# Optimization experiments

Measured on AMD Instinct MI355X. Metric: run time of the kernel, lower is better.

## Reference

```python
import jax, jax.numpy as jnp
import numpy as np

B, T, F, H, E = 256, 512, 32, 512, 32
NUM_TICKERS, PREDICT_DAYS = 5000, 30


def setup_inputs() -> dict:
    key = jax.random.key(0)
    ks = jax.random.split(key, 16)
    s = 0.05  # small init scale for stability
    return {
        "ticker_id": jax.random.randint(ks[0], (B,), 0, NUM_TICKERS),
        "sequence": jax.random.normal(ks[1], (B, T, F), jnp.float32),
        "embed_table": jax.random.normal(ks[2], (NUM_TICKERS, E), jnp.float32) * s,
        "Wih0": jax.random.normal(ks[3], (3 * H, F), jnp.float32) * s,
        "Whh0": jax.random.normal(ks[4], (3 * H, H), jnp.float32) * s,
        "bih0": jax.random.normal(ks[5], (3 * H,), jnp.float32) * s,
        "bhh0": jax.random.normal(ks[6], (3 * H,), jnp.float32) * s,
        "Wih1": jax.random.normal(ks[7], (3 * H, H), jnp.float32) * s,
        "Whh1": jax.random.normal(ks[8], (3 * H, H), jnp.float32) * s,
        "bih1": jax.random.normal(ks[9], (3 * H,), jnp.float32) * s,
        "bhh1": jax.random.normal(ks[10], (3 * H,), jnp.float32) * s,
        "fc1_w": jax.random.normal(ks[11], (H, H + E), jnp.float32) * s,
        "fc1_b": jax.random.normal(ks[12], (H,), jnp.float32) * s,
        "fc2_w": jax.random.normal(ks[13], (PREDICT_DAYS, H), jnp.float32) * s,
        "fc2_b": jax.random.normal(ks[14], (PREDICT_DAYS,), jnp.float32) * s,
    }


def _gru_layer(x, Wih, Whh, bih, bhh):
    """Standard torch-convention GRU layer. x: (B,T,in) -> (B,T,H), h_last (B,H).
    Gate packing along 3H axis: [r, z, n]."""
    Hs = Whh.shape[1]
    # precompute input projections for all timesteps in one GEMM
    gx = jnp.einsum('btf,gf->tbg', x, Wih) + bih  # (T,B,3H)

    def step(h, gxt):
        gh = h @ Whh.T + bhh                         # (B,3H)
        r = jax.nn.sigmoid(gxt[:, :Hs] + gh[:, :Hs])
        z = jax.nn.sigmoid(gxt[:, Hs:2 * Hs] + gh[:, Hs:2 * Hs])
        n = jnp.tanh(gxt[:, 2 * Hs:] + r * gh[:, 2 * Hs:])
        h_new = (1.0 - z) * n + z * h
        return h_new, h_new

    h0 = jnp.zeros((x.shape[0], Hs), x.dtype)
    h_last, ys = jax.lax.scan(step, h0, gx)          # ys: (T,B,H)
    return jnp.moveaxis(ys, 0, 1), h_last


def reference(ticker_id, sequence, embed_table, Wih0, Whh0, bih0, bhh0,
              Wih1, Whh1, bih1, bhh1, fc1_w, fc1_b, fc2_w, fc2_b):
    out0, _ = _gru_layer(sequence, Wih0, Whh0, bih0, bhh0)
    _, h_last = _gru_layer(out0, Wih1, Whh1, bih1, bhh1)   # top-layer final hidden (B,H)
    embed = embed_table[ticker_id]                          # (B,E)
    h = jnp.concatenate([h_last, embed], axis=1)            # (B,H+E)
    h = jax.nn.relu(h @ fc1_w.T + fc1_b)                    # dropout is eval no-op
    return h @ fc2_w.T + fc2_b                              # (B, predict_days)
```

## Files before the change

### kernel.cpp

```cpp
#include <hip/hip_runtime.h>
#include <hip/hip_bf16.h>


namespace {
constexpr int kB  = 256;
constexpr int kT  = 512;
constexpr int kF  = 32;
constexpr int kH  = 512;
constexpr int kE  = 32;
constexpr int kPD = 30;

constexpr int GBLK = 256;
constexpr int NTHR = 256;
constexpr int RG   = 32;
constexpr int HB   = 16;

constexpr int IMG  = kB * kH * 2;
constexpr int RING = 8;

constexpr int PART_OFF = 0;
constexpr int MB_OFF   = 8192;
constexpr int LDSB     = 98304;
static_assert(LDSB <= 160 * 1024, "LDS overflow");

constexpr size_t WS_CNT   = 0;
constexpr size_t WS_TOTAL = 1024;
constexpr size_t WS_FB    = 1152;
constexpr size_t WS_FLG   = 2048;
constexpr size_t WS_H0B   = 65536;
constexpr size_t WS_H1B   = WS_H0B + (size_t)RING * IMG;
constexpr size_t WS_H1F   = WS_H1B + (size_t)RING * IMG;
constexpr size_t WS_INIT  = WS_H1F;

typedef __bf16 bf16_t;
typedef __bf16 bf16x8 __attribute__((ext_vector_type(8)));
typedef float  f32x4  __attribute__((ext_vector_type(4)));

#define MFMA __builtin_amdgcn_mfma_f32_16x16x32_bf16
#define LDSF4(p) (*(__attribute__((address_space(3))) f32x4*)(p))
#define LDSVU(p) (*(volatile __attribute__((address_space(3))) unsigned*)(p))

#define WAITVM(N)                                              \
  do {                                                         \
    asm volatile("s_waitcnt vmcnt(" #N ")" ::: "memory");      \
    __builtin_amdgcn_sched_barrier(0);                         \
  } while (0)

__device__ __forceinline__ float sigmoid_f(float x) {
  return 1.f / (1.f + __expf(-x));
}
__device__ __forceinline__ float tanh_f(float x) {
  float a = fabsf(x);
  float e = __expf(-2.f * a);
  float t = (1.f - e) / (1.f + e);
  return copysignf(t, x);
}

__device__ __forceinline__ bf16x8 ld16a(const char* p) {
  bf16x8 v;
  asm volatile("global_load_dwordx4 %0, %1, off"
               : "=v"(v) : "v"(p) : "memory");
  return v;
}

__device__ __forceinline__ bf16x8 fragf(const float* p) {
  bf16x8 t;
#pragma unroll
  for (int j = 0; j < 8; ++j) t[j] = (bf16_t)p[j];
  return t;
}

__device__ __forceinline__ bf16x8 ld16_mall(const bf16_t* p) {
  const unsigned long long* q = (const unsigned long long*)p;
  unsigned long long lo =
      __hip_atomic_load(q, __ATOMIC_RELAXED, __HIP_MEMORY_SCOPE_AGENT);
  unsigned long long hi =
      __hip_atomic_load(q + 1, __ATOMIC_RELAXED, __HIP_MEMORY_SCOPE_AGENT);
  union { unsigned long long u[2]; bf16x8 v; } x;
  x.u[0] = lo; x.u[1] = hi;
  return x.v;
}

__device__ __forceinline__ void st2_mall(bf16_t* p, float v) {
  bf16_t b = (bf16_t)v;
  unsigned short bits = __builtin_bit_cast(unsigned short, b);
  __hip_atomic_store((unsigned short*)p, bits, __ATOMIC_RELAXED,
                     __HIP_MEMORY_SCOPE_AGENT);
}
template <bool XL>
__device__ __forceinline__ void st2x(bf16_t* p, float v) {
  if constexpr (XL) *p = (bf16_t)v;
  else st2_mall(p, v);
}

__device__ __forceinline__ void drain_stores() {
  asm volatile("s_waitcnt vmcnt(0)" ::: "memory");
}

__device__ __forceinline__ void busy_fma(float* a) {
#pragma unroll
  for (int i = 0; i < 16; ++i) {
    asm volatile("v_fmac_f32 %0, %1, %2" : "+v"(a[0]) : "v"(a[1]), "v"(a[2]));
    asm volatile("v_fmac_f32 %0, %1, %2" : "+v"(a[1]) : "v"(a[2]), "v"(a[3]));
    asm volatile("v_fmac_f32 %0, %1, %2" : "+v"(a[2]) : "v"(a[3]), "v"(a[0]));
    asm volatile("v_fmac_f32 %0, %1, %2" : "+v"(a[3]) : "v"(a[0]), "v"(a[1]));
  }
}

__device__ __forceinline__ void mb_spin(unsigned* mbp, unsigned tgt,
                                        float* a) {
  long guard = 0;
  while (LDSVU(mbp) < tgt) {
    busy_fma(a);
    if (++guard > (1L << 20)) break;
  }
  asm volatile("" ::: "memory");
}

__device__ __forceinline__ unsigned ld_flag_sc1(const unsigned* p) {
  unsigned v;
  asm volatile("global_load_dword %0, %1, off sc1\n\ts_waitcnt vmcnt(0)"
               : "=v"(v) : "v"(p) : "memory");
  return v;
}

template <bool XL>
__device__ __forceinline__ void flag_store(unsigned* flgp, int slot,
                                           unsigned tgt) {
  if constexpr (XL) {
    *(volatile unsigned*)(flgp + slot) = tgt;
  } else {
    __hip_atomic_store(flgp + slot, tgt, __ATOMIC_RELAXED,
                       __HIP_MEMORY_SCOPE_AGENT);
  }
}

template <bool XL>
__device__ __forceinline__ void flag_poll(const unsigned* flgp, int lane,
                                          unsigned tgt) {
  const unsigned* fp = flgp + (lane & 31);
  long guard = 0;
  if constexpr (XL) {
    for (;;) {
      unsigned v = ld_flag_sc1(fp);
      if (__all((int)(v >= tgt))) break;
      if (++guard > (1L << 22)) break;
    }
  } else {
    for (;;) {
      unsigned v = __hip_atomic_load(fp, __ATOMIC_RELAXED,
                                     __HIP_MEMORY_SCOPE_AGENT);
      if (__all((int)(v >= tgt))) break;
      __builtin_amdgcn_s_sleep(1);
      if (++guard > (1L << 20)) break;
    }
  }
}
}


#define L0_ISSUE(buf, base)                                         \
  _Pragma("unroll") for (int j = 0; j < 4; ++j)                     \
      buf[j] = ld16a(hsrc + (base + j) * 1024)
#define L0_MFMA(buf, base)                                          \
  _Pragma("unroll") for (int j = 0; j < 4; ++j) {                   \
    aR  = MFMA(buf[j], f0[0][base + j], aR, 0, 0, 0);               \
    aZ  = MFMA(buf[j], f0[1][base + j], aZ, 0, 0, 0);               \
    aNH = MFMA(buf[j], f0[2][base + j], aNH, 0, 0, 0);              \
  }
#define L1_ISSUE(b0, b1, base)                                      \
  _Pragma("unroll") for (int j = 0; j < 4; ++j) {                   \
    b0[j] = ld16a(hsrc + (base + j) * 1024);                        \
    b1[j] = ld16a(hsrc + 16384 + (base + j) * 1024);                \
  }
#define L1_MFMA(acc0, acc1, acc2, w, b0, b1, base)                  \
  _Pragma("unroll") for (int j = 0; j < 4; ++j) {                   \
    acc0[0] = MFMA(b0[j], w[0][base + j], acc0[0], 0, 0, 0);        \
    acc0[1] = MFMA(b1[j], w[0][base + j], acc0[1], 0, 0, 0);        \
    acc1[0] = MFMA(b0[j], w[1][base + j], acc1[0], 0, 0, 0);        \
    acc1[1] = MFMA(b1[j], w[1][base + j], acc1[1], 0, 0, 0);        \
    acc2[0] = MFMA(b0[j], w[2][base + j], acc2[0], 0, 0, 0);        \
    acc2[1] = MFMA(b1[j], w[2][base + j], acc2[1], 0, 0, 0);        \
  }

template <bool XL>
__device__ __attribute__((noinline)) void role_l0(
    const float* __restrict__ seq, const float* __restrict__ Whh0,
    const float* __restrict__ Wih0, bf16_t* __restrict__ h0b,
    unsigned* mbp, int g, int slot, int lane, int rbase, int rt, int c,
    float b0r, float b0z, float b0nx, float b0nh) {
  const int lm = lane & 15, lq = lane >> 4, koff = lq * 8;
  const int arow = rbase + rt * 16 + lm;

  bf16x8 f0[3][17];
#pragma unroll
  for (int gg = 0; gg < 3; ++gg) {
    const float* wh = Whh0 + (size_t)(gg * kH + c) * kH + koff;
#pragma unroll
    for (int kc = 0; kc < 16; ++kc) f0[gg][kc] = fragf(wh + kc * 32);
    f0[gg][16] = fragf(Wih0 + (size_t)(gg * kH + c) * kF + koff);
  }
  float h0m[4] = {0.f, 0.f, 0.f, 0.f};
  float spin[4] = {1.0f + lane, 0.5f, 0.25f, 0.125f};

  const int kcb = slot >> 1;
  const int lq2 = ((slot & 1) << 1) | (lm >> 3);
  const int stoff = ((g * 2 + rt) * 16 + kcb) * 1024 +
                    ((lq2 << 4) + lq * 4) * 16 + (lm & 7) * 2;
  const int tbase = (g * 2 + rt) * 16 * 1024;

  for (int s = 0; s <= kT; ++s) {
    const int pr = (s + RING - 1) & (RING - 1), pw = s & (RING - 1);
    if (s < kT) {
      f32x4 aR{0,0,0,0}, aZ{0,0,0,0}, aNH{0,0,0,0}, aNX{0,0,0,0};
      const char* hsrc = (const char*)h0b + pr * IMG + tbase + lane * 16;
      const float* xp = seq + ((size_t)arow * kT + s) * kF + koff;
      float xs[8];
#pragma unroll
      for (int j = 0; j < 8; ++j) xs[j] = xp[j];
      if constexpr (XL) {
        bf16x8 cA[4], cB[4];
        L0_ISSUE(cA, 0);
        L0_ISSUE(cB, 4);
        WAITVM(4);
        L0_MFMA(cA, 0);
        L0_ISSUE(cA, 8);
        WAITVM(4);
        L0_MFMA(cB, 4);
        L0_ISSUE(cB, 12);
        WAITVM(4);
        L0_MFMA(cA, 8);
        WAITVM(0);
        L0_MFMA(cB, 12);
      } else {
#pragma unroll
        for (int kc = 0; kc < 16; ++kc) {
          bf16x8 a = ld16_mall((const bf16_t*)(hsrc + kc * 1024));
          aR  = MFMA(a, f0[0][kc], aR, 0, 0, 0);
          aZ  = MFMA(a, f0[1][kc], aZ, 0, 0, 0);
          aNH = MFMA(a, f0[2][kc], aNH, 0, 0, 0);
        }
      }
      {
        bf16x8 ax;
#pragma unroll
        for (int j = 0; j < 8; ++j) ax[j] = (bf16_t)xs[j];
        aR  = MFMA(ax, f0[0][16], aR, 0, 0, 0);
        aZ  = MFMA(ax, f0[1][16], aZ, 0, 0, 0);
        aNX = MFMA(ax, f0[2][16], aNX, 0, 0, 0);
      }
      char* hnb = (char*)h0b + pw * IMG;
#pragma unroll
      for (int i = 0; i < 4; ++i) {
        float r = sigmoid_f(aR[i] + b0r);
        float z = sigmoid_f(aZ[i] + b0z);
        float n = tanh_f((aNX[i] + b0nx) + r * (aNH[i] + b0nh));
        float hn = (1.f - z) * n + z * h0m[i];
        h0m[i] = hn;
        st2x<XL>((bf16_t*)(hnb + stoff + i * 16), hn);
      }
    }
    __syncthreads();
    if constexpr (XL) {
      if (s < kT) mb_spin(mbp, (unsigned)(s + 1), spin);
    } else {
      __syncthreads();
    }
  }
}

template <bool XL>
__device__ __attribute__((noinline)) void role_l1h(
    const float* __restrict__ Whh1, bf16_t* __restrict__ h1b,
    float* __restrict__ h1f, unsigned* __restrict__ flgp, int slot,
    float* part, unsigned* mbp, int g, int lane, int rbase, int c,
    float b1r, float b1z, float b1nx, float b1nh) {
  const int lm = lane & 15, lq = lane >> 4, koff = lq * 8;
  bf16x8 fh[3][16];
#pragma unroll
  for (int gg = 0; gg < 3; ++gg) {
    const float* wh = Whh1 + (size_t)(gg * kH + c) * kH + koff;
#pragma unroll
    for (int kc = 0; kc < 16; ++kc) fh[gg][kc] = fragf(wh + kc * 32);
  }
  float h1m[2][4] = {{0,0,0,0},{0,0,0,0}};

  const int kcb = slot >> 1;
  const int lq2 = ((slot & 1) << 1) | (lm >> 3);
  const int st0 = (g * 2 * 16 + kcb) * 1024 +
                  ((lq2 << 4) + lq * 4) * 16 + (lm & 7) * 2;
  const int tbase = g * 2 * 16 * 1024;

  for (int s = 0; s <= kT; ++s) {
    const int pr = (s + RING - 1) & (RING - 1), pw = s & (RING - 1);
    f32x4 cR[2], cZ[2], cNH[2];
#pragma unroll
    for (int rt = 0; rt < 2; ++rt) {
      cR[rt] = f32x4{0,0,0,0}; cZ[rt] = f32x4{0,0,0,0}; cNH[rt] = f32x4{0,0,0,0};
    }
    if (s >= 1) {
      const char* hsrc = (const char*)h1b + pr * IMG + tbase + lane * 16;
      if constexpr (XL) {
        bf16x8 a0A[4], a1A[4], a0B[4], a1B[4];
        L1_ISSUE(a0A, a1A, 0);
        L1_ISSUE(a0B, a1B, 4);
        WAITVM(8);
        L1_MFMA(cR, cZ, cNH, fh, a0A, a1A, 0);
        L1_ISSUE(a0A, a1A, 8);
        WAITVM(8);
        L1_MFMA(cR, cZ, cNH, fh, a0B, a1B, 4);
        L1_ISSUE(a0B, a1B, 12);
        WAITVM(8);
        L1_MFMA(cR, cZ, cNH, fh, a0A, a1A, 8);
        WAITVM(0);
        L1_MFMA(cR, cZ, cNH, fh, a0B, a1B, 12);
      } else {
#pragma unroll
        for (int kc = 0; kc < 16; ++kc) {
          bf16x8 a0 = ld16_mall((const bf16_t*)(hsrc + kc * 1024));
          bf16x8 a1 = ld16_mall((const bf16_t*)(hsrc + 16384 + kc * 1024));
          cR[0]  = MFMA(a0, fh[0][kc], cR[0], 0,0,0);
          cR[1]  = MFMA(a1, fh[0][kc], cR[1], 0,0,0);
          cZ[0]  = MFMA(a0, fh[1][kc], cZ[0], 0,0,0);
          cZ[1]  = MFMA(a1, fh[1][kc], cZ[1], 0,0,0);
          cNH[0] = MFMA(a0, fh[2][kc], cNH[0],0,0,0);
          cNH[1] = MFMA(a1, fh[2][kc], cNH[1],0,0,0);
        }
      }
    }
    __syncthreads();
    if (s >= 1) {
      char* hnb = (char*)h1b + pw * IMG;
#pragma unroll
      for (int rt = 0; rt < 2; ++rt) {
        f32x4 pR  = LDSF4(part + ((rt * 3 + 0) * 64 + lane) * 4);
        f32x4 pZ  = LDSF4(part + ((rt * 3 + 1) * 64 + lane) * 4);
        f32x4 pNX = LDSF4(part + ((rt * 3 + 2) * 64 + lane) * 4);
#pragma unroll
        for (int i = 0; i < 4; ++i) {
          float r = sigmoid_f(cR[rt][i] + pR[i] + b1r);
          float z = sigmoid_f(cZ[rt][i] + pZ[i] + b1z);
          float n = tanh_f((pNX[i] + b1nx) + r * (cNH[rt][i] + b1nh));
          float hn = (1.f - z) * n + z * h1m[rt][i];
          h1m[rt][i] = hn;
          if (s < kT) st2x<XL>((bf16_t*)(hnb + st0 + rt * 16384 + i * 16), hn);
          else        h1f[(rbase + rt * 16 + lq * 4 + i) * kH + c] = hn;
        }
      }
    }
    if constexpr (XL) {
      if (s < kT) {
        drain_stores();
        if (lane == 0) flag_store<XL>(flgp, slot, (unsigned)(s + 1));
        flag_poll<XL>(flgp, lane, (unsigned)(s + 1));
        if ((s & (RING - 1)) == (RING - 1))
          asm volatile("buffer_inv" ::: "memory");
        if (lane == 0) LDSVU(mbp) = (unsigned)(s + 1);
      }
    } else {
      if (s < kT) {
        drain_stores();
        if (lane == 0) flag_store<XL>(flgp, slot, (unsigned)(s + 1));
        flag_poll<XL>(flgp, lane, (unsigned)(s + 1));
      }
      __syncthreads();
    }
  }
}

template <bool XL>
__device__ __attribute__((noinline)) void role_l1x(
    const float* __restrict__ Wih1, bf16_t* __restrict__ h0b,
    float* part, unsigned* mbp, int g, int lane, int c) {
  const int lq = lane >> 4, koff = lq * 8;
  bf16x8 fx[3][16];
#pragma unroll
  for (int gg = 0; gg < 3; ++gg) {
    const float* wi = Wih1 + (size_t)(gg * kH + c) * kH + koff;
#pragma unroll
    for (int kc = 0; kc < 16; ++kc) fx[gg][kc] = fragf(wi + kc * 32);
  }
  const int tbase = g * 2 * 16 * 1024;
  float spin[4] = {3.0f + lane, 0.5f, 0.25f, 0.125f};

  for (int s = 0; s <= kT; ++s) {
    const int pr = (s + RING - 1) & (RING - 1);
    if (s >= 1) {
      f32x4 xR[2], xZ[2], xNX[2];
#pragma unroll
      for (int rt = 0; rt < 2; ++rt) {
        xR[rt] = f32x4{0,0,0,0}; xZ[rt] = f32x4{0,0,0,0}; xNX[rt] = f32x4{0,0,0,0};
      }
      const char* hsrc = (const char*)h0b + pr * IMG + tbase + lane * 16;
      if constexpr (XL) {
        bf16x8 a0A[4], a1A[4], a0B[4], a1B[4];
        L1_ISSUE(a0A, a1A, 0);
        L1_ISSUE(a0B, a1B, 4);
        WAITVM(8);
        L1_MFMA(xR, xZ, xNX, fx, a0A, a1A, 0);
        L1_ISSUE(a0A, a1A, 8);
        WAITVM(8);
        L1_MFMA(xR, xZ, xNX, fx, a0B, a1B, 4);
        L1_ISSUE(a0B, a1B, 12);
        WAITVM(8);
        L1_MFMA(xR, xZ, xNX, fx, a0A, a1A, 8);
        WAITVM(0);
        L1_MFMA(xR, xZ, xNX, fx, a0B, a1B, 12);
      } else {
#pragma unroll
        for (int kc = 0; kc < 16; ++kc) {
          bf16x8 a0 = ld16_mall((const bf16_t*)(hsrc + kc * 1024));
          bf16x8 a1 = ld16_mall((const bf16_t*)(hsrc + 16384 + kc * 1024));
          xR[0]  = MFMA(a0, fx[0][kc], xR[0], 0,0,0);
          xR[1]  = MFMA(a1, fx[0][kc], xR[1], 0,0,0);
          xZ[0]  = MFMA(a0, fx[1][kc], xZ[0], 0,0,0);
          xZ[1]  = MFMA(a1, fx[1][kc], xZ[1], 0,0,0);
          xNX[0] = MFMA(a0, fx[2][kc], xNX[0],0,0,0);
          xNX[1] = MFMA(a1, fx[2][kc], xNX[1],0,0,0);
        }
      }
#pragma unroll
      for (int rt = 0; rt < 2; ++rt) {
        LDSF4(part + ((rt * 3 + 0) * 64 + lane) * 4) = xR[rt];
        LDSF4(part + ((rt * 3 + 1) * 64 + lane) * 4) = xZ[rt];
        LDSF4(part + ((rt * 3 + 2) * 64 + lane) * 4) = xNX[rt];
      }
    }
    __syncthreads();
    if constexpr (XL) {
      if (s < kT) mb_spin(mbp, (unsigned)(s + 1), spin);
    } else {
      __syncthreads();
    }
  }
}

__launch_bounds__(NTHR, 1)
__global__ void gru_persistent(
    const float* __restrict__ seq,
    const float* __restrict__ Wih0, const float* __restrict__ Whh0,
    const float* __restrict__ bih0, const float* __restrict__ bhh0,
    const float* __restrict__ Wih1, const float* __restrict__ Whh1,
    const float* __restrict__ bih1, const float* __restrict__ bhh1,
    char* __restrict__ ws) {
  extern __shared__ char smem[];
  float* part = (float*)(smem + PART_OFF);
  unsigned* mbp = (unsigned*)(smem + MB_OFF);
  __shared__ unsigned sh_enc;

  const int tid = threadIdx.x;

  if (tid == 0) {
    LDSVU(mbp) = 0u;
    unsigned xcd;
    asm("s_getreg_b32 %0, hwreg(HW_REG_XCC_ID)" : "=s"(xcd));
    xcd &= 7;
    unsigned* cnt   = (unsigned*)(ws + WS_CNT) + xcd * 32;
    unsigned* total = (unsigned*)(ws + WS_TOTAL);
    unsigned* fb    = (unsigned*)(ws + WS_FB);
    unsigned slot = __hip_atomic_fetch_add(cnt, 1u, __ATOMIC_RELAXED,
                                           __HIP_MEMORY_SCOPE_AGENT);
    if (slot >= 32)
      __hip_atomic_store(fb, 1u, __ATOMIC_RELAXED, __HIP_MEMORY_SCOPE_AGENT);
    __hip_atomic_fetch_add(total, 1u, __ATOMIC_RELAXED,
                           __HIP_MEMORY_SCOPE_AGENT);
    long guard = 0;
    while (__hip_atomic_load(total, __ATOMIC_RELAXED,
                             __HIP_MEMORY_SCOPE_AGENT) < (unsigned)GBLK) {
      __builtin_amdgcn_s_sleep(1);
      if (++guard > (1L << 24)) break;
    }
    unsigned f = __hip_atomic_load(fb, __ATOMIC_RELAXED,
                                   __HIP_MEMORY_SCOPE_AGENT);
    sh_enc = (f << 31) | (xcd << 8) | (slot & 255);
  }
  __syncthreads();
  const unsigned enc = sh_enc;
  const bool fallback = (enc >> 31) != 0;
  const int g    = fallback ? (blockIdx.x & 7)  : (int)((enc >> 8) & 7);
  const int slot = fallback ? (blockIdx.x >> 3) : (int)(enc & 255);
  const int hs   = slot * HB;

  const int lm = tid & 15;
  const int c = hs + lm;
  const float b0r  = bih0[c] + bhh0[c];
  const float b0z  = bih0[kH + c] + bhh0[kH + c];
  const float b0nx = bih0[2 * kH + c];
  const float b0nh = bhh0[2 * kH + c];
  const float b1r  = bih1[c] + bhh1[c];
  const float b1z  = bih1[kH + c] + bhh1[kH + c];
  const float b1nx = bih1[2 * kH + c];
  const float b1nh = bhh1[2 * kH + c];

  bf16_t* h0b = (bf16_t*)(ws + WS_H0B);
  bf16_t* h1b = (bf16_t*)(ws + WS_H1B);
  float*  h1f = (float*)(ws + WS_H1F);
  unsigned* flgp = (unsigned*)(ws + WS_FLG) + g * 32;
  const int wv   = tid >> 6;
  const int lane = tid & 63;
  const int rbase = g * RG;

  if (!fallback) {
    if (wv == 0)
      role_l0<true>(seq, Whh0, Wih0, h0b, mbp, g, slot, lane, rbase, 0, c,
                    b0r, b0z, b0nx, b0nh);
    else if (wv == 2)
      role_l0<true>(seq, Whh0, Wih0, h0b, mbp, g, slot, lane, rbase, 1, c,
                    b0r, b0z, b0nx, b0nh);
    else if (wv == 1)
      role_l1h<true>(Whh1, h1b, h1f, flgp, slot, part, mbp, g, lane, rbase,
                     c, b1r, b1z, b1nx, b1nh);
    else
      role_l1x<true>(Wih1, h0b, part, mbp, g, lane, c);
  } else {
    if (wv == 0)
      role_l0<false>(seq, Whh0, Wih0, h0b, mbp, g, slot, lane, rbase, 0, c,
                     b0r, b0z, b0nx, b0nh);
    else if (wv == 2)
      role_l0<false>(seq, Whh0, Wih0, h0b, mbp, g, slot, lane, rbase, 1, c,
                     b0r, b0z, b0nx, b0nh);
    else if (wv == 1)
      role_l1h<false>(Whh1, h1b, h1f, flgp, slot, part, mbp, g, lane, rbase,
                      c, b1r, b1z, b1nx, b1nh);
    else
      role_l1x<false>(Wih1, h0b, part, mbp, g, lane, c);
  }
}

__global__ void head_kernel(const float* __restrict__ h1,
                            const int* __restrict__ ticker,
                            const float* __restrict__ etab,
                            const float* __restrict__ fc1w,
                            const float* __restrict__ fc1b,
                            const float* __restrict__ fc2w,
                            const float* __restrict__ fc2b,
                            float* __restrict__ out) {
  __shared__ float xin[4][kH + kE];
  __shared__ float y1[4][kH];
  const int tid = threadIdx.x;
  const int b0 = blockIdx.x * 4;

  for (int idx = tid; idx < 4 * (kH + kE); idx += 256) {
    const int r = idx / (kH + kE), k = idx % (kH + kE);
    const int b = b0 + r;
    xin[r][k] = (k < kH) ? h1[b * kH + k] : etab[ticker[b] * kE + (k - kH)];
  }
  __syncthreads();

#pragma unroll
  for (int jj = 0; jj < 2; ++jj) {
    const int j = tid + jj * 256;
    const float* wr = fc1w + j * (kH + kE);
    float a0 = 0.f, a1 = 0.f, a2 = 0.f, a3 = 0.f;
    for (int k = 0; k < kH + kE; ++k) {
      const float w = wr[k];
      a0 += w * xin[0][k];
      a1 += w * xin[1][k];
      a2 += w * xin[2][k];
      a3 += w * xin[3][k];
    }
    const float bb = fc1b[j];
    y1[0][j] = fmaxf(a0 + bb, 0.f);
    y1[1][j] = fmaxf(a1 + bb, 0.f);
    y1[2][j] = fmaxf(a2 + bb, 0.f);
    y1[3][j] = fmaxf(a3 + bb, 0.f);
  }
  __syncthreads();

  if (tid < 4 * kPD) {
    const int r = tid / kPD, j = tid % kPD;
    const float* wr = fc2w + j * kH;
    float acc = fc2b[j];
    for (int k = 0; k < kH; ++k) acc += wr[k] * y1[r][k];
    out[(b0 + r) * kPD + j] = acc;
  }
}

extern "C" void kernel_launch(void* const* d_in, const int* in_sizes, int n_in,
                              void* d_out, int out_size, void* d_ws,
                              size_t ws_size, hipStream_t stream) {
  (void)in_sizes; (void)n_in; (void)out_size; (void)ws_size;

  const int*   ticker = (const int*)d_in[0];
  const float* seq    = (const float*)d_in[1];
  const float* etab   = (const float*)d_in[2];
  const float* Wih0   = (const float*)d_in[3];
  const float* Whh0   = (const float*)d_in[4];
  const float* bih0   = (const float*)d_in[5];
  const float* bhh0   = (const float*)d_in[6];
  const float* Wih1   = (const float*)d_in[7];
  const float* Whh1   = (const float*)d_in[8];
  const float* bih1   = (const float*)d_in[9];
  const float* bhh1   = (const float*)d_in[10];
  const float* fc1w   = (const float*)d_in[11];
  const float* fc1b   = (const float*)d_in[12];
  const float* fc2w   = (const float*)d_in[13];
  const float* fc2b   = (const float*)d_in[14];

  char* ws = (char*)d_ws;
  (void)hipMemsetAsync(ws, 0, WS_INIT, stream);

  gru_persistent<<<GBLK, NTHR, LDSB, stream>>>(
      seq, Wih0, Whh0, bih0, bhh0, Wih1, Whh1, bih1, bhh1, ws);

  head_kernel<<<kB / 4, 256, 0, stream>>>((const float*)(ws + WS_H1F), ticker,
                                          etab, fc1w, fc1b, fc2w, fc2b,
                                          (float*)d_out);
}
```

Measured before the change: 2.502 ms.

## Decouple layer-0 and layer-1 waves with per-layer global flags and double-buffered partials

```diff
diff --git a/kernel.cpp b/kernel.cpp
--- a/kernel.cpp
+++ b/kernel.cpp
@@ -19,14 +19,15 @@
 constexpr int RING = 8;
 
 constexpr int PART_OFF = 0;
-constexpr int MB_OFF   = 8192;
+constexpr int PARTN    = 1536;
 constexpr int LDSB     = 98304;
 static_assert(LDSB <= 160 * 1024, "LDS overflow");
 
 constexpr size_t WS_CNT   = 0;
 constexpr size_t WS_TOTAL = 1024;
 constexpr size_t WS_FB    = 1152;
-constexpr size_t WS_FLG   = 2048;
+constexpr size_t WS_FLG1  = 2048;
+constexpr size_t WS_FLG0  = 4096;
 constexpr size_t WS_H0B   = 65536;
 constexpr size_t WS_H1B   = WS_H0B + (size_t)RING * IMG;
 constexpr size_t WS_H1F   = WS_H1B + (size_t)RING * IMG;
@@ -38,7 +39,6 @@
 
 #define MFMA __builtin_amdgcn_mfma_f32_16x16x32_bf16
 #define LDSF4(p) (*(__attribute__((address_space(3))) f32x4*)(p))
-#define LDSVU(p) (*(volatile __attribute__((address_space(3))) unsigned*)(p))
 
 #define WAITVM(N)                                              \
   do {                                                         \
@@ -97,52 +97,21 @@
   asm volatile("s_waitcnt vmcnt(0)" ::: "memory");
 }
 
-__device__ __forceinline__ void busy_fma(float* a) {
-#pragma unroll
-  for (int i = 0; i < 16; ++i) {
-    asm volatile("v_fmac_f32 %0, %1, %2" : "+v"(a[0]) : "v"(a[1]), "v"(a[2]));
-    asm volatile("v_fmac_f32 %0, %1, %2" : "+v"(a[1]) : "v"(a[2]), "v"(a[3]));
-    asm volatile("v_fmac_f32 %0, %1, %2" : "+v"(a[2]) : "v"(a[3]), "v"(a[0]));
-    asm volatile("v_fmac_f32 %0, %1, %2" : "+v"(a[3]) : "v"(a[0]), "v"(a[1]));
-  }
-}
-
-__device__ __forceinline__ void mb_spin(unsigned* mbp, unsigned tgt,
-                                        float* a) {
-  long guard = 0;
-  while (LDSVU(mbp) < tgt) {
-    busy_fma(a);
-    if (++guard > (1L << 20)) break;
-  }
-  asm volatile("" ::: "memory");
-}
-
-__device__ __forceinline__ unsigned ld_flag_sc1(const unsigned* p) {
-  unsigned v;
-  asm volatile("global_load_dword %0, %1, off sc1\n\ts_waitcnt vmcnt(0)"
-               : "=v"(v) : "v"(p) : "memory");
+__device__ __forceinline__ unsigned atomic_rd_l2(const unsigned* p) {
+  unsigned v, z = 0;
+  asm volatile("global_atomic_add %0, %1, %2, off sc0\n\ts_waitcnt vmcnt(0)"
+               : "=v"(v) : "v"(p), "v"(z) : "memory");
   return v;
 }
 
 template <bool XL>
-__device__ __forceinline__ void flag_store(unsigned* flgp, int slot,
+__device__ __forceinline__ void poll_flags(const unsigned* base, int idx,
                                            unsigned tgt) {
-  if constexpr (XL) {
-    *(volatile unsigned*)(flgp + slot) = tgt;
-  } else {
-    __hip_atomic_store(flgp + slot, tgt, __ATOMIC_RELAXED,
-                       __HIP_MEMORY_SCOPE_AGENT);
-  }
-}
-
-template <bool XL>
-__device__ __forceinline__ void flag_poll(const unsigned* flgp, int lane,
-                                          unsigned tgt) {
-  const unsigned* fp = flgp + (lane & 31);
+  const unsigned* fp = base + idx;
   long guard = 0;
   if constexpr (XL) {
     for (;;) {
-      unsigned v = ld_flag_sc1(fp);
+      unsigned v = atomic_rd_l2(fp);
       if (__all((int)(v >= tgt))) break;
       if (++guard > (1L << 22)) break;
     }
@@ -154,6 +123,15 @@
       __builtin_amdgcn_s_sleep(1);
       if (++guard > (1L << 20)) break;
     }
+  }
+}
+
+template <bool XL>
+__device__ __forceinline__ void flag_post(unsigned* p, unsigned tgt) {
+  if constexpr (XL) {
+    *(volatile unsigned*)p = tgt;
+  } else {
+    __hip_atomic_store(p, tgt, __ATOMIC_RELAXED, __HIP_MEMORY_SCOPE_AGENT);
   }
 }
 }
@@ -187,8 +165,8 @@
 __device__ __attribute__((noinline)) void role_l0(
     const float* __restrict__ seq, const float* __restrict__ Whh0,
     const float* __restrict__ Wih0, bf16_t* __restrict__ h0b,
-    unsigned* mbp, int g, int slot, int lane, int rbase, int rt, int c,
-    float b0r, float b0z, float b0nx, float b0nh) {
+    unsigned* __restrict__ flg0p, int g, int slot, int lane, int rbase,
+    int rt, int c, float b0r, float b0z, float b0nx, float b0nh) {
   const int lm = lane & 15, lq = lane >> 4, koff = lq * 8;
   const int arow = rbase + rt * 16 + lm;
 
@@ -201,7 +179,6 @@
     f0[gg][16] = fragf(Wih0 + (size_t)(gg * kH + c) * kF + koff);
   }
   float h0m[4] = {0.f, 0.f, 0.f, 0.f};
-  float spin[4] = {1.0f + lane, 0.5f, 0.25f, 0.125f};
 
   const int kcb = slot >> 1;
   const int lq2 = ((slot & 1) << 1) | (lm >> 3);
@@ -212,12 +189,16 @@
   for (int s = 0; s <= kT; ++s) {
     const int pr = (s + RING - 1) & (RING - 1), pw = s & (RING - 1);
     if (s < kT) {
+      const float* xp = seq + ((size_t)arow * kT + s) * kF + koff;
+      float xs[8];
+#pragma unroll
+      for (int j = 0; j < 8; ++j) xs[j] = xp[j];
+      if (s > 0) poll_flags<XL>(flg0p, lane, (unsigned)s);
+      if constexpr (XL) {
+        if ((s & (RING - 1)) == 0) asm volatile("buffer_inv" ::: "memory");
+      }
       f32x4 aR{0,0,0,0}, aZ{0,0,0,0}, aNH{0,0,0,0}, aNX{0,0,0,0};
       const char* hsrc = (const char*)h0b + pr * IMG + tbase + lane * 16;
-      const float* xp = seq + ((size_t)arow * kT + s) * kF + koff;
-      float xs[8];
-#pragma unroll
-      for (int j = 0; j < 8; ++j) xs[j] = xp[j];
       if constexpr (XL) {
         bf16x8 cA[4], cB[4];
         L0_ISSUE(cA, 0);
@@ -259,21 +240,19 @@
         h0m[i] = hn;
         st2x<XL>((bf16_t*)(hnb + stoff + i * 16), hn);
       }
+      drain_stores();
+      if (lane == 0) flag_post<XL>(flg0p + rt * 32 + slot, (unsigned)(s + 1));
     }
     __syncthreads();
-    if constexpr (XL) {
-      if (s < kT) mb_spin(mbp, (unsigned)(s + 1), spin);
-    } else {
-      __syncthreads();
-    }
+    if constexpr (!XL) __syncthreads();
   }
 }
 
 template <bool XL>
 __device__ __attribute__((noinline)) void role_l1h(
     const float* __restrict__ Whh1, bf16_t* __restrict__ h1b,
-    float* __restrict__ h1f, unsigned* __restrict__ flgp, int slot,
-    float* part, unsigned* mbp, int g, int lane, int rbase, int c,
+    float* __restrict__ h1f, unsigned* __restrict__ flg1p, int slot,
+    float* part, int g, int lane, int rbase, int c,
     float b1r, float b1z, float b1nx, float b1nh) {
   const int lm = lane & 15, lq = lane >> 4, koff = lq * 8;
   bf16x8 fh[3][16];
@@ -299,6 +278,10 @@
       cR[rt] = f32x4{0,0,0,0}; cZ[rt] = f32x4{0,0,0,0}; cNH[rt] = f32x4{0,0,0,0};
     }
     if (s >= 1) {
+      poll_flags<XL>(flg1p, lane & 31, (unsigned)s);
+      if constexpr (XL) {
+        if ((s & (RING - 1)) == 0) asm volatile("buffer_inv" ::: "memory");
+      }
       const char* hsrc = (const char*)h1b + pr * IMG + tbase + lane * 16;
       if constexpr (XL) {
         bf16x8 a0A[4], a1A[4], a0B[4], a1B[4];
@@ -330,12 +313,13 @@
     }
     __syncthreads();
     if (s >= 1) {
+      float* pb = part + (s & 1) * PARTN;
       char* hnb = (char*)h1b + pw * IMG;
 #pragma unroll
       for (int rt = 0; rt < 2; ++rt) {
-        f32x4 pR  = LDSF4(part + ((rt * 3 + 0) * 64 + lane) * 4);
-        f32x4 pZ  = LDSF4(part + ((rt * 3 + 1) * 64 + lane) * 4);
-        f32x4 pNX = LDSF4(part + ((rt * 3 + 2) * 64 + lane) * 4);
+        f32x4 pR  = LDSF4(pb + ((rt * 3 + 0) * 64 + lane) * 4);
+        f32x4 pZ  = LDSF4(pb + ((rt * 3 + 1) * 64 + lane) * 4);
+        f32x4 pNX = LDSF4(pb + ((rt * 3 + 2) * 64 + lane) * 4);
 #pragma unroll
         for (int i = 0; i < 4; ++i) {
           float r = sigmoid_f(cR[rt][i] + pR[i] + b1r);
@@ -348,21 +332,12 @@
         }
       }
     }
-    if constexpr (XL) {
-      if (s < kT) {
-        drain_stores();
-        if (lane == 0) flag_store<XL>(flgp, slot, (unsigned)(s + 1));
-        flag_poll<XL>(flgp, lane, (unsigned)(s + 1));
-        if ((s & (RING - 1)) == (RING - 1))
-          asm volatile("buffer_inv" ::: "memory");
-        if (lane == 0) LDSVU(mbp) = (unsigned)(s + 1);
-      }
-    } else {
-      if (s < kT) {
-        drain_stores();
-        if (lane == 0) flag_store<XL>(flgp, slot, (unsigned)(s + 1));
-        flag_poll<XL>(flgp, lane, (unsigned)(s + 1));
-      }
+    if (s < kT) {
+      drain_stores();
+      if (lane == 0) flag_post<XL>(flg1p + slot, (unsigned)(s + 1));
+    }
+    if constexpr (!XL) {
+      if (s < kT) poll_flags<XL>(flg1p, lane & 31, (unsigned)(s + 1));
       __syncthreads();
     }
   }
@@ -371,7 +346,7 @@
 template <bool XL>
 __device__ __attribute__((noinline)) void role_l1x(
     const float* __restrict__ Wih1, bf16_t* __restrict__ h0b,
-    float* part, unsigned* mbp, int g, int lane, int c) {
+    float* part, unsigned* __restrict__ flg0p, int g, int lane, int c) {
   const int lq = lane >> 4, koff = lq * 8;
   bf16x8 fx[3][16];
 #pragma unroll
@@ -381,11 +356,14 @@
     for (int kc = 0; kc < 16; ++kc) fx[gg][kc] = fragf(wi + kc * 32);
   }
   const int tbase = g * 2 * 16 * 1024;
-  float spin[4] = {3.0f + lane, 0.5f, 0.25f, 0.125f};
 
   for (int s = 0; s <= kT; ++s) {
     const int pr = (s + RING - 1) & (RING - 1);
     if (s >= 1) {
+      poll_flags<XL>(flg0p, lane, (unsigned)s);
+      if constexpr (XL) {
+        if ((s & (RING - 1)) == 0) asm volatile("buffer_inv" ::: "memory");
+      }
       f32x4 xR[2], xZ[2], xNX[2];
 #pragma unroll
       for (int rt = 0; rt < 2; ++rt) {
@@ -419,19 +397,16 @@
           xNX[1] = MFMA(a1, fx[2][kc], xNX[1],0,0,0);
         }
       }
+      float* pb = part + (s & 1) * PARTN;
 #pragma unroll
       for (int rt = 0; rt < 2; ++rt) {
-        LDSF4(part + ((rt * 3 + 0) * 64 + lane) * 4) = xR[rt];
-        LDSF4(part + ((rt * 3 + 1) * 64 + lane) * 4) = xZ[rt];
-        LDSF4(part + ((rt * 3 + 2) * 64 + lane) * 4) = xNX[rt];
+        LDSF4(pb + ((rt * 3 + 0) * 64 + lane) * 4) = xR[rt];
+        LDSF4(pb + ((rt * 3 + 1) * 64 + lane) * 4) = xZ[rt];
+        LDSF4(pb + ((rt * 3 + 2) * 64 + lane) * 4) = xNX[rt];
       }
     }
     __syncthreads();
-    if constexpr (XL) {
-      if (s < kT) mb_spin(mbp, (unsigned)(s + 1), spin);
-    } else {
-      __syncthreads();
-    }
+    if constexpr (!XL) __syncthreads();
   }
 }
 
@@ -445,13 +420,11 @@
     char* __restrict__ ws) {
   extern __shared__ char smem[];
   float* part = (float*)(smem + PART_OFF);
-  unsigned* mbp = (unsigned*)(smem + MB_OFF);
   __shared__ unsigned sh_enc;
 
   const int tid = threadIdx.x;
 
   if (tid == 0) {
-    LDSVU(mbp) = 0u;
     unsigned xcd;
     asm("s_getreg_b32 %0, hwreg(HW_REG_XCC_ID)" : "=s"(xcd));
     xcd &= 7;
@@ -495,35 +468,36 @@
   bf16_t* h0b = (bf16_t*)(ws + WS_H0B);
   bf16_t* h1b = (bf16_t*)(ws + WS_H1B);
   float*  h1f = (float*)(ws + WS_H1F);
-  unsigned* flgp = (unsigned*)(ws + WS_FLG) + g * 32;
+  unsigned* flg1p = (unsigned*)(ws + WS_FLG1) + g * 32;
+  unsigned* flg0p = (unsigned*)(ws + WS_FLG0) + g * 64;
   const int wv   = tid >> 6;
   const int lane = tid & 63;
   const int rbase = g * RG;
 
   if (!fallback) {
     if (wv == 0)
-      role_l0<true>(seq, Whh0, Wih0, h0b, mbp, g, slot, lane, rbase, 0, c,
+      role_l0<true>(seq, Whh0, Wih0, h0b, flg0p, g, slot, lane, rbase, 0, c,
                     b0r, b0z, b0nx, b0nh);
     else if (wv == 2)
-      role_l0<true>(seq, Whh0, Wih0, h0b, mbp, g, slot, lane, rbase, 1, c,
+      role_l0<true>(seq, Whh0, Wih0, h0b, flg0p, g, slot, lane, rbase, 1, c,
                     b0r, b0z, b0nx, b0nh);
     else if (wv == 1)
-      role_l1h<true>(Whh1, h1b, h1f, flgp, slot, part, mbp, g, lane, rbase,
-                     c, b1r, b1z, b1nx, b1nh);
+      role_l1h<true>(Whh1, h1b, h1f, flg1p, slot, part, g, lane, rbase, c,
+                     b1r, b1z, b1nx, b1nh);
     else
-      role_l1x<true>(Wih1, h0b, part, mbp, g, lane, c);
+      role_l1x<true>(Wih1, h0b, part, flg0p, g, lane, c);
   } else {
     if (wv == 0)
-      role_l0<false>(seq, Whh0, Wih0, h0b, mbp, g, slot, lane, rbase, 0, c,
+      role_l0<false>(seq, Whh0, Wih0, h0b, flg0p, g, slot, lane, rbase, 0, c,
                      b0r, b0z, b0nx, b0nh);
     else if (wv == 2)
-      role_l0<false>(seq, Whh0, Wih0, h0b, mbp, g, slot, lane, rbase, 1, c,
+      role_l0<false>(seq, Whh0, Wih0, h0b, flg0p, g, slot, lane, rbase, 1, c,
                      b0r, b0z, b0nx, b0nh);
     else if (wv == 1)
-      role_l1h<false>(Whh1, h1b, h1f, flgp, slot, part, mbp, g, lane, rbase,
-                      c, b1r, b1z, b1nx, b1nh);
+      role_l1h<false>(Whh1, h1b, h1f, flg1p, slot, part, g, lane, rbase, c,
+                      b1r, b1z, b1nx, b1nh);
     else
-      role_l1x<false>(Wih1, h0b, part, mbp, g, lane, c);
+      role_l1x<false>(Wih1, h0b, part, flg0p, g, lane, c);
   }
 }
 
```

After: 5.824 ms. 133% more time.
